# Performance work log

Measured on AMD Instinct MI355X. Metric: run time of the kernel, lower is better.

## Reference

```python
import jax, jax.numpy as jnp
import numpy as np

D_MODEL = 256
N_HEADS = 4
WINDOW = 8
DECAY = 0.9
STEP_SIZE = 0.5


def _linear(x, w, b):
    # torch nn.Linear: y = x @ w.T + b, w: [out, in]
    return jnp.einsum('...i,oi->...o', x, w) + b


def _layernorm(x, scale, bias, eps=1e-5):
    mu = jnp.mean(x, axis=-1, keepdims=True)
    var = jnp.var(x, axis=-1, keepdims=True)
    return (x - mu) * jax.lax.rsqrt(var + eps) * scale + bias


def _ema(x, decay):
    # ema[t] = decay*ema[t-1] + (1-decay)*x[t], ema[-1]=0
    # (exactly the causal conv with weights (1-d)*d^i from the torch code)
    def step(c, xt):
        c = decay * c + (1.0 - decay) * xt
        return c, c
    _, ys = jax.lax.scan(step, jnp.zeros_like(x[:, 0]), jnp.swapaxes(x, 0, 1))
    return jnp.swapaxes(ys, 0, 1)


def setup_inputs() -> dict:
    key = jax.random.key(0)
    ks = iter(jax.random.split(key, 40))
    B, T, D = 8, 1024, D_MODEL
    s = 0.02
    inp = {
        'parallel_repr': jax.random.normal(next(ks), (B, T, D), jnp.float32),
        'sequential_state': jax.random.normal(next(ks), (B, D), jnp.float32),
        'trajectory_summary': jax.random.normal(next(ks), (B, D), jnp.float32),
        # MultiheadAttention params
        'in_proj_w': jax.random.normal(next(ks), (3 * D, D), jnp.float32) * s,
        'in_proj_b': jnp.zeros((3 * D,), jnp.float32),
        'out_proj_w': jax.random.normal(next(ks), (D, D), jnp.float32) * s,
        'out_proj_b': jnp.zeros((D,), jnp.float32),
        # depthwise causal conv (local history)
        'conv_w': jax.random.normal(next(ks), (D, 1, WINDOW), jnp.float32) * s,
        'conv_b': jnp.zeros((D,), jnp.float32),
        # parallel_to_sequential / sequential_to_parallel
        'p2s_w': jax.random.normal(next(ks), (D, D), jnp.float32) * s,
        'p2s_b': jnp.zeros((D,), jnp.float32),
        's2p_w': jax.random.normal(next(ks), (D, D), jnp.float32) * s,
        's2p_b': jnp.zeros((D,), jnp.float32),
        # transition MLP: 3D -> 2D -> D
        'trans_w1': jax.random.normal(next(ks), (2 * D, 3 * D), jnp.float32) * s,
        'trans_b1': jnp.zeros((2 * D,), jnp.float32),
        'trans_w2': jax.random.normal(next(ks), (D, 2 * D), jnp.float32) * s,
        'trans_b2': jnp.zeros((D,), jnp.float32),
        # FFN: D -> 4D -> D
        'ffn_w1': jax.random.normal(next(ks), (4 * D, D), jnp.float32) * s,
        'ffn_b1': jnp.zeros((4 * D,), jnp.float32),
        'ffn_w2': jax.random.normal(next(ks), (D, 4 * D), jnp.float32) * s,
        'ffn_b2': jnp.zeros((D,), jnp.float32),
        # LayerNorms
        'ln1_s': jnp.ones((D,), jnp.float32), 'ln1_b': jnp.zeros((D,), jnp.float32),
        'ln2_s': jnp.ones((D,), jnp.float32), 'ln2_b': jnp.zeros((D,), jnp.float32),
        'ln3_s': jnp.ones((D,), jnp.float32), 'ln3_b': jnp.zeros((D,), jnp.float32),
        'ln4_s': jnp.ones((D,), jnp.float32), 'ln4_b': jnp.zeros((D,), jnp.float32),
    }
    return inp


def _forward(parallel_repr, sequential_state,
             in_proj_w, in_proj_b, out_proj_w, out_proj_b,
             conv_w, conv_b, p2s_w, p2s_b, s2p_w, s2p_b,
             trans_w1, trans_b1, trans_w2, trans_b2,
             ffn_w1, ffn_b1, ffn_w2, ffn_b2,
             ln1_s, ln1_b, ln2_s, ln2_b, ln3_s, ln3_b, ln4_s, ln4_b):
    B, T, D = parallel_repr.shape
    H, hd = N_HEADS, D // N_HEADS

    # --- causal self-attention (nn.MultiheadAttention, batch_first) ---
    qkv = _linear(parallel_repr, in_proj_w, in_proj_b)
    q, k, v = jnp.split(qkv, 3, axis=-1)
    q = q.reshape(B, T, H, hd)
    k = k.reshape(B, T, H, hd)
    v = v.reshape(B, T, H, hd)
    scores = jnp.einsum('bqhd,bkhd->bhqk', q, k) / jnp.sqrt(jnp.asarray(hd, q.dtype))
    causal = jnp.triu(jnp.ones((T, T), bool), 1)
    scores = jnp.where(causal, jnp.finfo(scores.dtype).min, scores)
    attn = jax.nn.softmax(scores, axis=-1)
    attn_out = jnp.einsum('bhqk,bkhd->bqhd', attn, v).reshape(B, T, D)
    attn_out = _linear(attn_out, out_proj_w, out_proj_b)
    x = _layernorm(parallel_repr + attn_out, ln1_s, ln1_b)

    # --- depthwise causal conv (local history) ---
    xt = jnp.swapaxes(x, 1, 2)  # [B, D, T]
    xt_pad = jnp.pad(xt, ((0, 0), (0, 0), (WINDOW - 1, 0)))
    local = jax.lax.conv_general_dilated(
        xt_pad, conv_w, window_strides=(1,), padding='VALID',
        dimension_numbers=('NCH', 'OIH', 'NCH'), feature_group_count=D)
    local_history = jnp.swapaxes(local + conv_b[None, :, None], 1, 2)  # [B, T, D]

    # --- global EMA summary ---
    global_summary = _ema(x, DECAY)

    # --- transition deltas + cumsum state integration ---
    parallel_guidance = _linear(x, p2s_w, p2s_b)
    combined = jnp.concatenate([x + 0.3 * parallel_guidance, local_history, global_summary], axis=-1)
    h = jax.nn.gelu(_linear(combined, trans_w1, trans_b1), approximate=False)
    deltas = _linear(h, trans_w2, trans_b2)
    states = sequential_state[:, None, :] + jnp.cumsum(deltas, axis=1) * STEP_SIZE
    states = _layernorm(states, ln3_s, ln3_b)

    # --- FFN with sequential guidance ---
    seq_guidance = _linear(states, s2p_w, s2p_b)
    f = jax.nn.gelu(_linear(x + 0.3 * seq_guidance, ffn_w1, ffn_b1), approximate=False)
    ffn_out = _linear(f, ffn_w2, ffn_b2)
    x = _layernorm(x + ffn_out, ln2_s, ln2_b)

    final_sequential_state = _layernorm(states[:, -1, :], ln4_s, ln4_b)
    final_trajectory_summary = global_summary[:, -1, :]
    return x, final_sequential_state, final_trajectory_summary


def reference(parallel_repr, sequential_state, trajectory_summary,
              in_proj_w, in_proj_b, out_proj_w, out_proj_b,
              conv_w, conv_b, p2s_w, p2s_b, s2p_w, s2p_b,
              trans_w1, trans_b1, trans_w2, trans_b2,
              ffn_w1, ffn_b1, ffn_w2, ffn_b2,
              ln1_s, ln1_b, ln2_s, ln2_b, ln3_s, ln3_b, ln4_s, ln4_b):
    # trajectory_summary is accepted by the torch forward but never used.
    return _forward(parallel_repr, sequential_state,
                    in_proj_w, in_proj_b, out_proj_w, out_proj_b,
                    conv_w, conv_b, p2s_w, p2s_b, s2p_w, s2p_b,
                    trans_w1, trans_b1, trans_w2, trans_b2,
                    ffn_w1, ffn_b1, ffn_w2, ffn_b2,
                    ln1_s, ln1_b, ln2_s, ln2_b, ln3_s, ln3_b, ln4_s, ln4_b)
```

## Files before the change

kernel.cpp:

```cpp
#include <hip/hip_runtime.h>
#include <math.h>

typedef unsigned short u16;
typedef __attribute__((ext_vector_type(8))) short bf16x8;
typedef __attribute__((ext_vector_type(4))) float f32x4;

#define D_MODEL 256
#define T_SZ 1024
constexpr size_t S_ELT = (size_t)8192 * 256;
constexpr size_t MB = 1024 * 1024;

constexpr size_t OFF_QKV = 0;
constexpr size_t OFF_ATTN = 12 * MB;
constexpr size_t OFF_F = 0;
constexpr size_t OFF_X = 16 * MB;
constexpr size_t OFF_COMB = 24 * MB;
constexpr size_t OFF_FB = 36 * MB;
constexpr size_t OFF_H = 44 * MB;
constexpr size_t OFF_XBF = 48 * MB;
constexpr size_t OFF_WB = 52 * MB;
constexpr size_t OFF_SCR1 = 55 * MB;
constexpr size_t OFF_SCR2 = 55 * MB + 262144;

constexpr int WB_INPROJ = 0;
constexpr int WB_OUTPROJ = 196608;
constexpr int WB_P2S = 262144;
constexpr int WB_S2P = 327680;
constexpr int WB_T1 = 393216;
constexpr int WB_T2 = 786432;
constexpr int WB_F1 = 917504;
constexpr int WB_F2 = 1179648;
constexpr int WB_TOTAL = 1441792;

__device__ __forceinline__ u16 f2bf(float f) {
  unsigned int u = __float_as_uint(f);
  u += 0x7fff + ((u >> 16) & 1);
  return (u16)(u >> 16);
}
__device__ __forceinline__ float bf2f(u16 s) {
  return __uint_as_float(((unsigned int)s) << 16);
}

__device__ __forceinline__ void glds16(const u16* g, u16* l) {
  __builtin_amdgcn_global_load_lds(
      (const __attribute__((address_space(1))) void*)g,
      (__attribute__((address_space(3))) void*)l, 16, 0, 0);
}

__global__ __launch_bounds__(256)
void wconv_kernel(const float* w0, const float* w1, const float* w2,
                  const float* w3, const float* w4, const float* w5,
                  const float* w6, const float* w7, u16* __restrict__ outp) {
  const int idx4 = (blockIdx.x * 256 + threadIdx.x) * 4;
  if (idx4 >= WB_TOTAL) return;
  const int offs[9] = {WB_INPROJ, WB_OUTPROJ, WB_P2S,  WB_S2P, WB_T1,
                       WB_T2,     WB_F1,      WB_F2,   WB_TOTAL};
  const float* srcs[8] = {w0, w1, w2, w3, w4, w5, w6, w7};
  int seg = 0;
  while (idx4 >= offs[seg + 1]) ++seg;
  float4 v = *(const float4*)(srcs[seg] + (idx4 - offs[seg]));
  unsigned int lo = (unsigned int)f2bf(v.x) | ((unsigned int)f2bf(v.y) << 16);
  unsigned int hi = (unsigned int)f2bf(v.z) | ((unsigned int)f2bf(v.w) << 16);
  *(uint2*)(outp + idx4) = make_uint2(lo, hi);
}

__global__ __launch_bounds__(256)
void cvtbf_kernel(const float* __restrict__ src, u16* __restrict__ dst) {
  const int i4 = (blockIdx.x * 256 + threadIdx.x) * 4;
  float4 v = *(const float4*)(src + i4);
  unsigned int lo = (unsigned int)f2bf(v.x) | ((unsigned int)f2bf(v.y) << 16);
  unsigned int hi = (unsigned int)f2bf(v.z) | ((unsigned int)f2bf(v.w) << 16);
  *(uint2*)(dst + i4) = make_uint2(lo, hi);
}

enum { EPI_NONE = 0, EPI_GELU = 1, EPI_ADDSCALE = 2 };

template <int EPI, int BM, int BN, bool OUTBF>
__global__ __launch_bounds__(256)
void mgemm(const u16* __restrict__ A, int lda,
           const u16* __restrict__ Wb, int K, const float* __restrict__ bias,
           void* __restrict__ Cv, int ldc, int col_off,
           const float* __restrict__ addsrc) {
  __shared__ u16 As[BM * 32];
  __shared__ u16 Bs[BN * 32];
  const int tid = threadIdx.x;
  const int w = tid >> 6, lane = tid & 63;
  const int ln = lane & 15, quad = lane >> 4;
  const int m0 = blockIdx.x * BM;
  const int n0 = blockIdx.y * BN;
  constexpr int MT = (BM == 128 && BN == 128) ? 4 : (BM == 128 ? 2 : 1);
  const int wm = (BM == 128 && BN == 128) ? (w >> 1) * 64
                 : (BM == 128)            ? w * 32
                                          : w * 16;
  const int wn = (BM == 128 && BN == 128) ? (w & 1) * 64 : 0;
  constexpr int APW = BM / 64;
  constexpr int BPW = BN / 64;

  f32x4 acc[MT][4] = {};

  const int grow = lane >> 2;
  const int gk8 = (lane & 3) * 8;

  for (int k0 = 0; k0 < K; k0 += 32) {
#pragma unroll
    for (int p = 0; p < APW; ++p) {
      const int g = w * APW + p;
      glds16(A + (size_t)(m0 + g * 16 + grow) * lda + k0 + gk8, As + g * 512);
    }
#pragma unroll
    for (int p = 0; p < BPW; ++p) {
      const int g = w * BPW + p;
      glds16(Wb + (size_t)(n0 + g * 16 + grow) * K + k0 + gk8, Bs + g * 512);
    }
    __syncthreads();

    const u16* abase = As + (wm >> 4) * 512 + ln * 32 + quad * 8;
    const u16* bbase = Bs + (wn >> 4) * 512 + ln * 32 + quad * 8;
    bf16x8 af[MT], bv[4];
#pragma unroll
    for (int i = 0; i < MT; ++i) af[i] = *(const bf16x8*)(abase + i * 512);
#pragma unroll
    for (int j = 0; j < 4; ++j) bv[j] = *(const bf16x8*)(bbase + j * 512);
#pragma unroll
    for (int i = 0; i < MT; ++i)
#pragma unroll
      for (int j = 0; j < 4; ++j)
        acc[i][j] =
            __builtin_amdgcn_mfma_f32_16x16x32_bf16(af[i], bv[j], acc[i][j], 0, 0, 0);
    __syncthreads();
  }

#pragma unroll
  for (int i = 0; i < MT; ++i)
#pragma unroll
    for (int j = 0; j < 4; ++j) {
      const int col = n0 + wn + j * 16 + ln;
      const float bsv = bias[col];
#pragma unroll
      for (int r = 0; r < 4; ++r) {
        const int row = m0 + wm + i * 16 + quad * 4 + r;
        float v = acc[i][j][r] + bsv;
        if (EPI == EPI_GELU) v = 0.5f * v * (1.0f + erff(v * 0.70710678f));
        if (EPI == EPI_ADDSCALE) v = addsrc[(size_t)row * 256 + col] + 0.3f * v;
        if (OUTBF)
          ((u16*)Cv)[(size_t)row * ldc + col_off + col] = f2bf(v);
        else
          ((float*)Cv)[(size_t)row * ldc + col_off + col] = v;
      }
    }
}

__global__ __launch_bounds__(256)
void vtr_kernel(const u16* __restrict__ qkv, u16* __restrict__ vt) {
  __shared__ u16 Ls[64][66];
  const int tid = threadIdx.x;
  const int t0 = blockIdx.x * 64;
  const int bh = blockIdx.y;
  const int b = bh >> 2, h = bh & 3;
  const int r0 = tid >> 3, c8 = (tid & 7) * 8;
#pragma unroll
  for (int p = 0; p < 2; ++p) {
    const int t = t0 + r0 + p * 32;
    *(uint4*)&Ls[r0 + p * 32][c8] =
        *(const uint4*)(qkv + (size_t)(b * T_SZ + t) * 768 + 512 + h * 64 + c8);
  }
  __syncthreads();
#pragma unroll
  for (int p = 0; p < 2; ++p) {
    const int d = r0 + p * 32;
    union { u16 h16[8]; uint4 u; } pk;
#pragma unroll
    for (int e = 0; e < 8; ++e) pk.h16[e] = Ls[c8 + e][d];
    *(uint4*)(vt + (size_t)(bh * 64 + d) * T_SZ + t0 + c8) = pk.u;
  }
}

__global__ __launch_bounds__(256)
void attn_flash(const u16* __restrict__ qkv, const u16* __restrict__ vt,
                u16* __restrict__ outp) {
  __shared__ u16 Ps[4][16][72];
  const int tid = threadIdx.x;
  const int w = tid >> 6, lane = tid & 63;
  const int ln = lane & 15, quad = lane >> 4, kq8 = quad * 8;
  const int wu = blockIdx.x * 4 + w;
  const int bh = wu >> 6, s = wu & 63;
  const int qt = (s & 1) ? (63 - (s >> 1)) : (s >> 1);
  const int q0 = qt * 16;
  const int b = bh >> 2, h = bh & 3;
  const u16* base = qkv + (size_t)b * T_SZ * 768;
  const u16* vbase = vt + (size_t)bh * 64 * T_SZ;

  bf16x8 qf[2];
#pragma unroll
  for (int ks = 0; ks < 2; ++ks)
    qf[ks] = *(const bf16x8*)(base + (size_t)(q0 + ln) * 768 + h * 64 +
                              ks * 32 + kq8);
  const short ob = (short)0x3F80;
  const bf16x8 ones = {ob, ob, ob, ob, ob, ob, ob, ob};

  f32x4 O[4] = {};
  f32x4 l_acc = {};
  const int ntiles = (qt >> 2) + 1;
  for (int jt = 0; jt < ntiles; ++jt) {
    const int c0 = jt * 64;
    f32x4 sv[4] = {};
#pragma unroll
    for (int ks = 0; ks < 2; ++ks)
#pragma unroll
      for (int j = 0; j < 4; ++j) {
        bf16x8 kf = *(const bf16x8*)(base + (size_t)(c0 + j * 16 + ln) * 768 +
                                     256 + h * 64 + ks * 32 + kq8);
        sv[j] = __builtin_amdgcn_mfma_f32_16x16x32_bf16(qf[ks], kf, sv[j], 0, 0, 0);
      }
    const bool need_mask = (c0 + 63 > q0);
#pragma unroll
    for (int j = 0; j < 4; ++j)
#pragma unroll
      for (int r = 0; r < 4; ++r) {
        float p = __expf(sv[j][r] * 0.125f);
        if (need_mask && (c0 + j * 16 + ln > q0 + quad * 4 + r)) p = 0.f;
        Ps[w][quad * 4 + r][j * 16 + ln] = f2bf(p);
      }
#pragma unroll
    for (int ks = 0; ks < 2; ++ks) {
      bf16x8 pf = *(const bf16x8*)&Ps[w][ln][ks * 32 + kq8];
      l_acc = __builtin_amdgcn_mfma_f32_16x16x32_bf16(pf, ones, l_acc, 0, 0, 0);
#pragma unroll
      for (int j = 0; j < 4; ++j) {
        bf16x8 vf = *(const bf16x8*)(vbase + (size_t)(j * 16 + ln) * T_SZ +
                                     c0 + ks * 32 + kq8);
        O[j] = __builtin_amdgcn_mfma_f32_16x16x32_bf16(pf, vf, O[j], 0, 0, 0);
      }
    }
  }
  u16* op = outp + (size_t)b * T_SZ * 256;
#pragma unroll
  for (int r = 0; r < 4; ++r) {
    const float inv = 1.f / l_acc[r];
#pragma unroll
    for (int j = 0; j < 4; ++j)
      op[(size_t)(q0 + quad * 4 + r) * 256 + h * 64 + j * 16 + ln] =
          f2bf(O[j][r] * inv);
  }
}

__device__ __forceinline__ float block_reduce_sum(float v, float* tmp) {
#pragma unroll
  for (int o = 32; o > 0; o >>= 1) v += __shfl_down(v, o);
  const int lane = threadIdx.x & 63, wid = threadIdx.x >> 6;
  if (lane == 0) tmp[wid] = v;
  __syncthreads();
  v = tmp[0] + tmp[1] + tmp[2] + tmp[3];
  __syncthreads();
  return v;
}

__device__ __forceinline__ float ln_finish(float v, float s1, float s2,
                                           float g, float bb) {
  float mean = s1 * (1.f / 256.f);
  float var = s2 * (1.f / 256.f) - mean * mean;
  return (v - mean) * rsqrtf(var + 1e-5f) * g + bb;
}

__global__ __launch_bounds__(256)
void ln_add_kernel(const float* __restrict__ a, const float* __restrict__ addsrc,
                   const float* __restrict__ g, const float* __restrict__ bb,
                   float* __restrict__ outp, u16* __restrict__ obf) {
  __shared__ float tmp[4];
  const size_t row = blockIdx.x;
  const int d = threadIdx.x;
  float v = a[row * 256 + d] + addsrc[row * 256 + d];
  float s1 = block_reduce_sum(v, tmp);
  float s2 = block_reduce_sum(v * v, tmp);
  float y = ln_finish(v, s1, s2, g[d], bb[d]);
  outp[row * 256 + d] = y;
  if (obf) obf[row * 256 + d] = f2bf(y);
}

__global__ __launch_bounds__(256)
void ln3_states_kernel(const float* __restrict__ deltas, const float* __restrict__ scr,
                       const float* __restrict__ seq, const float* __restrict__ g,
                       const float* __restrict__ bb, u16* __restrict__ st) {
  __shared__ float tmp[4];
  const int row = blockIdx.x;
  const int b = row >> 10, t = row & 1023;
  const int d = threadIdx.x;
  float v = seq[b * 256 + d] +
            0.5f * (deltas[(size_t)row * 256 + d] +
                    scr[(size_t)(b * 32 + (t >> 5)) * 256 + d]);
  float s1 = block_reduce_sum(v, tmp);
  float s2 = block_reduce_sum(v * v, tmp);
  st[(size_t)row * 256 + d] = f2bf(ln_finish(v, s1, s2, g[d], bb[d]));
}

__global__ __launch_bounds__(256)
void ln4_kernel(const u16* __restrict__ st, const float* __restrict__ g,
                const float* __restrict__ bb, float* __restrict__ outp) {
  __shared__ float tmp[4];
  const int b = blockIdx.x, d = threadIdx.x;
  float v = bf2f(st[(size_t)(b * T_SZ + 1023) * 256 + d]);
  float s1 = block_reduce_sum(v, tmp);
  float s2 = block_reduce_sum(v * v, tmp);
  outp[b * 256 + d] = ln_finish(v, s1, s2, g[d], bb[d]);
}

__global__ __launch_bounds__(256)
void emaconv_kernel(const float* __restrict__ x, const float* __restrict__ cw,
                    const float* __restrict__ cb, u16* __restrict__ comb,
                    float* __restrict__ scr) {
  const int bc = blockIdx.x;
  const int b = bc >> 5, ch = bc & 31;
  const int d = threadIdx.x;
  const int t0 = ch * 32;
  float wreg[8];
#pragma unroll
  for (int j = 0; j < 8; ++j) wreg[j] = cw[d * 8 + j];
  const float bias = cb[d];
  float xw[8];
#pragma unroll
  for (int j = 0; j < 7; ++j) {
    const int ts = t0 - 7 + j;
    xw[j] = (ts >= 0) ? x[(size_t)(b * T_SZ + ts) * 256 + d] : 0.f;
  }
  float c = 0.f;
#pragma unroll
  for (int tl = 0; tl < 32; ++tl) {
    const size_t row = (size_t)(b * T_SZ + t0 + tl);
    xw[7] = x[row * 256 + d];
    float conv = bias;
#pragma unroll
    for (int j = 0; j < 8; ++j) conv = fmaf(xw[j], wreg[j], conv);
    c = 0.9f * c + 0.1f * xw[7];
    comb[row * 768 + 256 + d] = f2bf(conv);
    comb[row * 768 + 512 + d] = f2bf(c);
#pragma unroll
    for (int j = 0; j < 7; ++j) xw[j] = xw[j + 1];
  }
  scr[(size_t)bc * 256 + d] = c;
}

__global__ __launch_bounds__(256)
void ema_b_kernel(float* __restrict__ scr) {
  const int b = blockIdx.x, d = threadIdx.x;
  const float q32 = 0.03433683820292512f;
  float carry = 0.f;
  for (int ch = 0; ch < 32; ++ch) {
    const size_t idx = (size_t)(b * 32 + ch) * 256 + d;
    float e = scr[idx];
    scr[idx] = carry;
    carry = e + q32 * carry;
  }
}

__global__ __launch_bounds__(256)
void ema_c_kernel(u16* __restrict__ comb, const float* __restrict__ scr,
                  float* __restrict__ fts) {
  const int row = blockIdx.x;
  const int b = row >> 10, t = row & 1023;
  const int d = threadIdx.x;
  const int ch = t >> 5, tl = t & 31;
  float carry = scr[(size_t)(b * 32 + ch) * 256 + d];
  float l = bf2f(comb[(size_t)row * 768 + 512 + d]);
  float y = fmaf(__powf(0.9f, (float)(tl + 1)), carry, l);
  comb[(size_t)row * 768 + 512 + d] = f2bf(y);
  if (t == 1023) fts[b * 256 + d] = y;
}

__global__ __launch_bounds__(256)
void cs_a_kernel(float* __restrict__ deltas, float* __restrict__ scr) {
  const int bc = blockIdx.x;
  const int b = bc >> 5, ch = bc & 31;
  const int d = threadIdx.x;
  const int t0 = ch * 32;
  float c = 0.f;
  for (int tl = 0; tl < 32; ++tl) {
    const size_t idx = (size_t)(b * T_SZ + t0 + tl) * 256 + d;
    c += deltas[idx];
    deltas[idx] = c;
  }
  scr[(size_t)bc * 256 + d] = c;
}

__global__ __launch_bounds__(256)
void cs_b_kernel(float* __restrict__ scr) {
  const int b = blockIdx.x, d = threadIdx.x;
  float carry = 0.f;
  for (int ch = 0; ch < 32; ++ch) {
    const size_t idx = (size_t)(b * 32 + ch) * 256 + d;
    float e = scr[idx];
    scr[idx] = carry;
    carry += e;
  }
}

extern "C" void kernel_launch(void* const* d_in, const int* in_sizes, int n_in,
                              void* d_out, int out_size, void* d_ws,
                              size_t ws_size, hipStream_t stream) {
  (void)in_sizes; (void)n_in; (void)out_size; (void)ws_size;
  const float* parallel_repr = (const float*)d_in[0];
  const float* sequential_state = (const float*)d_in[1];
  const float* in_proj_b = (const float*)d_in[4];
  const float* out_proj_b = (const float*)d_in[6];
  const float* conv_w = (const float*)d_in[7];
  const float* conv_b = (const float*)d_in[8];
  const float* p2s_b = (const float*)d_in[10];
  const float* s2p_b = (const float*)d_in[12];
  const float* trans_b1 = (const float*)d_in[14];
  const float* trans_b2 = (const float*)d_in[16];
  const float* ffn_b1 = (const float*)d_in[18];
  const float* ffn_b2 = (const float*)d_in[20];
  const float* ln1_s = (const float*)d_in[21];
  const float* ln1_b = (const float*)d_in[22];
  const float* ln2_s = (const float*)d_in[23];
  const float* ln2_b = (const float*)d_in[24];
  const float* ln3_s = (const float*)d_in[25];
  const float* ln3_b = (const float*)d_in[26];
  const float* ln4_s = (const float*)d_in[27];
  const float* ln4_b = (const float*)d_in[28];

  char* ws = (char*)d_ws;
  u16* qkv_bf = (u16*)(ws + OFF_QKV);
  u16* attn_bf = (u16*)(ws + OFF_ATTN);
  u16* states_bf = (u16*)(ws + OFF_ATTN);
  u16* f_bf = (u16*)(ws + OFF_F);
  float* x = (float*)(ws + OFF_X);
  u16* comb = (u16*)(ws + OFF_COMB);
  u16* pr_bf = (u16*)(ws + OFF_COMB);
  u16* ffn_in = (u16*)(ws + OFF_COMB);
  float* fbuf = (float*)(ws + OFF_FB);
  u16* vt = (u16*)(ws + OFF_H);
  u16* h_bf = (u16*)(ws + OFF_H);
  u16* x_bf = (u16*)(ws + OFF_XBF);
  u16* wb = (u16*)(ws + OFF_WB);
  float* scr1 = (float*)(ws + OFF_SCR1);
  float* scr2 = (float*)(ws + OFF_SCR2);
  float* out = (float*)d_out;
  float* out_fss = out + S_ELT;
  float* out_fts = out + S_ELT + 2048;

  const dim3 blk(256);

  wconv_kernel<<<1408, blk, 0, stream>>>(
      (const float*)d_in[3], (const float*)d_in[5], (const float*)d_in[9],
      (const float*)d_in[11], (const float*)d_in[13], (const float*)d_in[15],
      (const float*)d_in[17], (const float*)d_in[19], wb);
  cvtbf_kernel<<<2048, blk, 0, stream>>>(parallel_repr, pr_bf);
  mgemm<EPI_NONE, 128, 128, true><<<dim3(64, 6), blk, 0, stream>>>(
      pr_bf, 256, wb + WB_INPROJ, 256, in_proj_b, qkv_bf, 768, 0, nullptr);
  vtr_kernel<<<dim3(16, 32), blk, 0, stream>>>(qkv_bf, vt);
  attn_flash<<<512, blk, 0, stream>>>(qkv_bf, vt, attn_bf);
  mgemm<EPI_NONE, 64, 64, false><<<dim3(128, 4), blk, 0, stream>>>(
      attn_bf, 256, wb + WB_OUTPROJ, 256, out_proj_b, fbuf, 256, 0, nullptr);
  ln_add_kernel<<<8192, blk, 0, stream>>>(parallel_repr, fbuf, ln1_s, ln1_b, x,
                                          x_bf);
  emaconv_kernel<<<256, blk, 0, stream>>>(x, conv_w, conv_b, comb, scr1);
  ema_b_kernel<<<8, blk, 0, stream>>>(scr1);
  ema_c_kernel<<<8192, blk, 0, stream>>>(comb, scr1, out_fts);
  mgemm<EPI_ADDSCALE, 64, 64, true><<<dim3(128, 4), blk, 0, stream>>>(
      x_bf, 256, wb + WB_P2S, 256, p2s_b, comb, 768, 0, x);
  mgemm<EPI_GELU, 128, 128, true><<<dim3(64, 4), blk, 0, stream>>>(
      comb, 768, wb + WB_T1, 768, trans_b1, h_bf, 512, 0, nullptr);
  mgemm<EPI_NONE, 64, 64, false><<<dim3(128, 4), blk, 0, stream>>>(
      h_bf, 512, wb + WB_T2, 512, trans_b2, fbuf, 256, 0, nullptr);
  cs_a_kernel<<<256, blk, 0, stream>>>(fbuf, scr2);
  cs_b_kernel<<<8, blk, 0, stream>>>(scr2);
  ln3_states_kernel<<<8192, blk, 0, stream>>>(fbuf, scr2, sequential_state,
                                              ln3_s, ln3_b, states_bf);
  ln4_kernel<<<8, blk, 0, stream>>>(states_bf, ln4_s, ln4_b, out_fss);
  mgemm<EPI_ADDSCALE, 64, 64, true><<<dim3(128, 4), blk, 0, stream>>>(
      states_bf, 256, wb + WB_S2P, 256, s2p_b, ffn_in, 256, 0, x);
  mgemm<EPI_GELU, 128, 128, true><<<dim3(64, 8), blk, 0, stream>>>(
      ffn_in, 256, wb + WB_F1, 256, ffn_b1, f_bf, 1024, 0, nullptr);
  mgemm<EPI_NONE, 64, 64, false><<<dim3(128, 4), blk, 0, stream>>>(
      f_bf, 1024, wb + WB_F2, 1024, ffn_b2, fbuf, 256, 0, nullptr);
  ln_add_kernel<<<8192, blk, 0, stream>>>(x, fbuf, ln2_s, ln2_b, out, nullptr);
}
```

Before: 303.3 us.

## Fuse conversions, write V transposed from QKV GEMM, deepen K tile

Merges the weight and input bf16 conversion kernels into one launch. The QKV GEMM epilogue now writes the V columns straight into the transposed layout, which removes the separate transpose kernel. The GEMM now stages K=64 per barrier instead of 32, halving the number of synchronisations, and drops the 128x128 tile in favour of 128x64 with more blocks and a min-occupancy launch bound. The transposed V store is a strided 8-byte write, so it may coalesce less well than the old transpose kernel, and the doubled LDS tiles can limit occupancy.

```diff
diff --git a/kernel.cpp b/kernel.cpp
--- a/kernel.cpp
+++ b/kernel.cpp
@@ -31,6 +31,7 @@
 constexpr int WB_F1 = 917504;
 constexpr int WB_F2 = 1179648;
 constexpr int WB_TOTAL = 1441792;
+constexpr int PR_TOTAL = 2097152;
 
 __device__ __forceinline__ u16 f2bf(float f) {
   unsigned int u = __float_as_uint(f);
@@ -50,49 +51,48 @@
 __global__ __launch_bounds__(256)
 void wconv_kernel(const float* w0, const float* w1, const float* w2,
                   const float* w3, const float* w4, const float* w5,
-                  const float* w6, const float* w7, u16* __restrict__ outp) {
+                  const float* w6, const float* w7, const float* pr,
+                  u16* __restrict__ wb, u16* __restrict__ prb) {
   const int idx4 = (blockIdx.x * 256 + threadIdx.x) * 4;
-  if (idx4 >= WB_TOTAL) return;
-  const int offs[9] = {WB_INPROJ, WB_OUTPROJ, WB_P2S,  WB_S2P, WB_T1,
-                       WB_T2,     WB_F1,      WB_F2,   WB_TOTAL};
-  const float* srcs[8] = {w0, w1, w2, w3, w4, w5, w6, w7};
-  int seg = 0;
-  while (idx4 >= offs[seg + 1]) ++seg;
-  float4 v = *(const float4*)(srcs[seg] + (idx4 - offs[seg]));
-  unsigned int lo = (unsigned int)f2bf(v.x) | ((unsigned int)f2bf(v.y) << 16);
-  unsigned int hi = (unsigned int)f2bf(v.z) | ((unsigned int)f2bf(v.w) << 16);
-  *(uint2*)(outp + idx4) = make_uint2(lo, hi);
-}
-
-__global__ __launch_bounds__(256)
-void cvtbf_kernel(const float* __restrict__ src, u16* __restrict__ dst) {
-  const int i4 = (blockIdx.x * 256 + threadIdx.x) * 4;
-  float4 v = *(const float4*)(src + i4);
-  unsigned int lo = (unsigned int)f2bf(v.x) | ((unsigned int)f2bf(v.y) << 16);
-  unsigned int hi = (unsigned int)f2bf(v.z) | ((unsigned int)f2bf(v.w) << 16);
-  *(uint2*)(dst + i4) = make_uint2(lo, hi);
+  if (idx4 < WB_TOTAL) {
+    const int offs[9] = {WB_INPROJ, WB_OUTPROJ, WB_P2S,  WB_S2P, WB_T1,
+                         WB_T2,     WB_F1,      WB_F2,   WB_TOTAL};
+    const float* srcs[8] = {w0, w1, w2, w3, w4, w5, w6, w7};
+    int seg = 0;
+    while (idx4 >= offs[seg + 1]) ++seg;
+    float4 v = *(const float4*)(srcs[seg] + (idx4 - offs[seg]));
+    unsigned int lo = (unsigned int)f2bf(v.x) | ((unsigned int)f2bf(v.y) << 16);
+    unsigned int hi = (unsigned int)f2bf(v.z) | ((unsigned int)f2bf(v.w) << 16);
+    *(uint2*)(wb + idx4) = make_uint2(lo, hi);
+  } else {
+    const int i4 = idx4 - WB_TOTAL;
+    if (i4 < PR_TOTAL) {
+      float4 v = *(const float4*)(pr + i4);
+      unsigned int lo = (unsigned int)f2bf(v.x) | ((unsigned int)f2bf(v.y) << 16);
+      unsigned int hi = (unsigned int)f2bf(v.z) | ((unsigned int)f2bf(v.w) << 16);
+      *(uint2*)(prb + i4) = make_uint2(lo, hi);
+    }
+  }
 }
 
 enum { EPI_NONE = 0, EPI_GELU = 1, EPI_ADDSCALE = 2 };
 
-template <int EPI, int BM, int BN, bool OUTBF>
-__global__ __launch_bounds__(256)
+template <int EPI, int BM, int BN, bool OUTBF, bool VSPLIT>
+__global__ __launch_bounds__(256, 4)
 void mgemm(const u16* __restrict__ A, int lda,
            const u16* __restrict__ Wb, int K, const float* __restrict__ bias,
            void* __restrict__ Cv, int ldc, int col_off,
-           const float* __restrict__ addsrc) {
-  __shared__ u16 As[BM * 32];
-  __shared__ u16 Bs[BN * 32];
+           const float* __restrict__ addsrc, u16* __restrict__ vt) {
+  __shared__ u16 As[BM * 64];
+  __shared__ u16 Bs[BN * 64];
   const int tid = threadIdx.x;
   const int w = tid >> 6, lane = tid & 63;
   const int ln = lane & 15, quad = lane >> 4;
   const int m0 = blockIdx.x * BM;
   const int n0 = blockIdx.y * BN;
-  constexpr int MT = (BM == 128 && BN == 128) ? 4 : (BM == 128 ? 2 : 1);
-  const int wm = (BM == 128 && BN == 128) ? (w >> 1) * 64
-                 : (BM == 128)            ? w * 32
-                                          : w * 16;
-  const int wn = (BM == 128 && BN == 128) ? (w & 1) * 64 : 0;
+  constexpr int MT = (BM == 128) ? 2 : 1;
+  const int wm = w * (MT * 16);
+  constexpr int wn = 0;
   constexpr int APW = BM / 64;
   constexpr int BPW = BN / 64;
 
@@ -101,32 +101,39 @@
   const int grow = lane >> 2;
   const int gk8 = (lane & 3) * 8;
 
-  for (int k0 = 0; k0 < K; k0 += 32) {
-#pragma unroll
-    for (int p = 0; p < APW; ++p) {
-      const int g = w * APW + p;
-      glds16(A + (size_t)(m0 + g * 16 + grow) * lda + k0 + gk8, As + g * 512);
-    }
-#pragma unroll
-    for (int p = 0; p < BPW; ++p) {
-      const int g = w * BPW + p;
-      glds16(Wb + (size_t)(n0 + g * 16 + grow) * K + k0 + gk8, Bs + g * 512);
+  for (int k0 = 0; k0 < K; k0 += 64) {
+#pragma unroll
+    for (int s = 0; s < 2; ++s) {
+#pragma unroll
+      for (int p = 0; p < APW; ++p) {
+        const int g = w * APW + p;
+        glds16(A + (size_t)(m0 + g * 16 + grow) * lda + k0 + s * 32 + gk8,
+               As + s * BM * 32 + g * 512);
+      }
+#pragma unroll
+      for (int p = 0; p < BPW; ++p) {
+        const int g = w * BPW + p;
+        glds16(Wb + (size_t)(n0 + g * 16 + grow) * K + k0 + s * 32 + gk8,
+               Bs + s * BN * 32 + g * 512);
+      }
     }
     __syncthreads();
-
-    const u16* abase = As + (wm >> 4) * 512 + ln * 32 + quad * 8;
-    const u16* bbase = Bs + (wn >> 4) * 512 + ln * 32 + quad * 8;
-    bf16x8 af[MT], bv[4];
-#pragma unroll
-    for (int i = 0; i < MT; ++i) af[i] = *(const bf16x8*)(abase + i * 512);
-#pragma unroll
-    for (int j = 0; j < 4; ++j) bv[j] = *(const bf16x8*)(bbase + j * 512);
-#pragma unroll
-    for (int i = 0; i < MT; ++i)
-#pragma unroll
-      for (int j = 0; j < 4; ++j)
-        acc[i][j] =
-            __builtin_amdgcn_mfma_f32_16x16x32_bf16(af[i], bv[j], acc[i][j], 0, 0, 0);
+#pragma unroll
+    for (int s = 0; s < 2; ++s) {
+      const u16* abase = As + s * BM * 32 + (wm >> 4) * 512 + ln * 32 + quad * 8;
+      const u16* bbase = Bs + s * BN * 32 + ln * 32 + quad * 8;
+      bf16x8 af[MT], bv[4];
+#pragma unroll
+      for (int i = 0; i < MT; ++i) af[i] = *(const bf16x8*)(abase + i * 512);
+#pragma unroll
+      for (int j = 0; j < 4; ++j) bv[j] = *(const bf16x8*)(bbase + j * 512);
+#pragma unroll
+      for (int i = 0; i < MT; ++i)
+#pragma unroll
+        for (int j = 0; j < 4; ++j)
+          acc[i][j] = __builtin_amdgcn_mfma_f32_16x16x32_bf16(af[i], bv[j],
+                                                              acc[i][j], 0, 0, 0);
+    }
     __syncthreads();
   }
 
@@ -136,43 +143,32 @@
     for (int j = 0; j < 4; ++j) {
       const int col = n0 + wn + j * 16 + ln;
       const float bsv = bias[col];
+      const int row0 = m0 + wm + i * 16 + quad * 4;
+      float vals[4];
 #pragma unroll
       for (int r = 0; r < 4; ++r) {
-        const int row = m0 + wm + i * 16 + quad * 4 + r;
         float v = acc[i][j][r] + bsv;
         if (EPI == EPI_GELU) v = 0.5f * v * (1.0f + erff(v * 0.70710678f));
-        if (EPI == EPI_ADDSCALE) v = addsrc[(size_t)row * 256 + col] + 0.3f * v;
-        if (OUTBF)
-          ((u16*)Cv)[(size_t)row * ldc + col_off + col] = f2bf(v);
-        else
-          ((float*)Cv)[(size_t)row * ldc + col_off + col] = v;
+        if (EPI == EPI_ADDSCALE)
+          v = addsrc[(size_t)(row0 + r) * 256 + col] + 0.3f * v;
+        vals[r] = v;
+      }
+      if (VSPLIT && col >= 512) {
+        ushort4 pk;
+        pk.x = f2bf(vals[0]); pk.y = f2bf(vals[1]);
+        pk.z = f2bf(vals[2]); pk.w = f2bf(vals[3]);
+        *(ushort4*)(vt + (size_t)((row0 >> 10) * 256 + (col - 512)) * T_SZ +
+                    (row0 & 1023)) = pk;
+      } else if (OUTBF) {
+#pragma unroll
+        for (int r = 0; r < 4; ++r)
+          ((u16*)Cv)[(size_t)(row0 + r) * ldc + col_off + col] = f2bf(vals[r]);
+      } else {
+#pragma unroll
+        for (int r = 0; r < 4; ++r)
+          ((float*)Cv)[(size_t)(row0 + r) * ldc + col_off + col] = vals[r];
       }
     }
-}
-
-__global__ __launch_bounds__(256)
-void vtr_kernel(const u16* __restrict__ qkv, u16* __restrict__ vt) {
-  __shared__ u16 Ls[64][66];
-  const int tid = threadIdx.x;
-  const int t0 = blockIdx.x * 64;
-  const int bh = blockIdx.y;
-  const int b = bh >> 2, h = bh & 3;
-  const int r0 = tid >> 3, c8 = (tid & 7) * 8;
-#pragma unroll
-  for (int p = 0; p < 2; ++p) {
-    const int t = t0 + r0 + p * 32;
-    *(uint4*)&Ls[r0 + p * 32][c8] =
-        *(const uint4*)(qkv + (size_t)(b * T_SZ + t) * 768 + 512 + h * 64 + c8);
-  }
-  __syncthreads();
-#pragma unroll
-  for (int p = 0; p < 2; ++p) {
-    const int d = r0 + p * 32;
-    union { u16 h16[8]; uint4 u; } pk;
-#pragma unroll
-    for (int e = 0; e < 8; ++e) pk.h16[e] = Ls[c8 + e][d];
-    *(uint4*)(vt + (size_t)(bh * 64 + d) * T_SZ + t0 + c8) = pk.u;
-  }
 }
 
 __global__ __launch_bounds__(256)
@@ -440,38 +436,37 @@
 
   const dim3 blk(256);
 
-  wconv_kernel<<<1408, blk, 0, stream>>>(
+  wconv_kernel<<<3456, blk, 0, stream>>>(
       (const float*)d_in[3], (const float*)d_in[5], (const float*)d_in[9],
       (const float*)d_in[11], (const float*)d_in[13], (const float*)d_in[15],
-      (const float*)d_in[17], (const float*)d_in[19], wb);
-  cvtbf_kernel<<<2048, blk, 0, stream>>>(parallel_repr, pr_bf);
-  mgemm<EPI_NONE, 128, 128, true><<<dim3(64, 6), blk, 0, stream>>>(
-      pr_bf, 256, wb + WB_INPROJ, 256, in_proj_b, qkv_bf, 768, 0, nullptr);
-  vtr_kernel<<<dim3(16, 32), blk, 0, stream>>>(qkv_bf, vt);
+      (const float*)d_in[17], (const float*)d_in[19], parallel_repr, wb, pr_bf);
+  mgemm<EPI_NONE, 128, 64, true, true><<<dim3(64, 12), blk, 0, stream>>>(
+      pr_bf, 256, wb + WB_INPROJ, 256, in_proj_b, qkv_bf, 768, 0, nullptr, vt);
   attn_flash<<<512, blk, 0, stream>>>(qkv_bf, vt, attn_bf);
-  mgemm<EPI_NONE, 64, 64, false><<<dim3(128, 4), blk, 0, stream>>>(
-      attn_bf, 256, wb + WB_OUTPROJ, 256, out_proj_b, fbuf, 256, 0, nullptr);
+  mgemm<EPI_NONE, 64, 64, false, false><<<dim3(128, 4), blk, 0, stream>>>(
+      attn_bf, 256, wb + WB_OUTPROJ, 256, out_proj_b, fbuf, 256, 0, nullptr,
+      nullptr);
   ln_add_kernel<<<8192, blk, 0, stream>>>(parallel_repr, fbuf, ln1_s, ln1_b, x,
                                           x_bf);
   emaconv_kernel<<<256, blk, 0, stream>>>(x, conv_w, conv_b, comb, scr1);
   ema_b_kernel<<<8, blk, 0, stream>>>(scr1);
   ema_c_kernel<<<8192, blk, 0, stream>>>(comb, scr1, out_fts);
-  mgemm<EPI_ADDSCALE, 64, 64, true><<<dim3(128, 4), blk, 0, stream>>>(
-      x_bf, 256, wb + WB_P2S, 256, p2s_b, comb, 768, 0, x);
-  mgemm<EPI_GELU, 128, 128, true><<<dim3(64, 4), blk, 0, stream>>>(
-      comb, 768, wb + WB_T1, 768, trans_b1, h_bf, 512, 0, nullptr);
-  mgemm<EPI_NONE, 64, 64, false><<<dim3(128, 4), blk, 0, stream>>>(
-      h_bf, 512, wb + WB_T2, 512, trans_b2, fbuf, 256, 0, nullptr);
+  mgemm<EPI_ADDSCALE, 64, 64, true, false><<<dim3(128, 4), blk, 0, stream>>>(
+      x_bf, 256, wb + WB_P2S, 256, p2s_b, comb, 768, 0, x, nullptr);
+  mgemm<EPI_GELU, 128, 64, true, false><<<dim3(64, 8), blk, 0, stream>>>(
+      comb, 768, wb + WB_T1, 768, trans_b1, h_bf, 512, 0, nullptr, nullptr);
+  mgemm<EPI_NONE, 64, 64, false, false><<<dim3(128, 4), blk, 0, stream>>>(
+      h_bf, 512, wb + WB_T2, 512, trans_b2, fbuf, 256, 0, nullptr, nullptr);
   cs_a_kernel<<<256, blk, 0, stream>>>(fbuf, scr2);
   cs_b_kernel<<<8, blk, 0, stream>>>(scr2);
   ln3_states_kernel<<<8192, blk, 0, stream>>>(fbuf, scr2, sequential_state,
                                               ln3_s, ln3_b, states_bf);
   ln4_kernel<<<8, blk, 0, stream>>>(states_bf, ln4_s, ln4_b, out_fss);
-  mgemm<EPI_ADDSCALE, 64, 64, true><<<dim3(128, 4), blk, 0, stream>>>(
-      states_bf, 256, wb + WB_S2P, 256, s2p_b, ffn_in, 256, 0, x);
-  mgemm<EPI_GELU, 128, 128, true><<<dim3(64, 8), blk, 0, stream>>>(
-      ffn_in, 256, wb + WB_F1, 256, ffn_b1, f_bf, 1024, 0, nullptr);
-  mgemm<EPI_NONE, 64, 64, false><<<dim3(128, 4), blk, 0, stream>>>(
-      f_bf, 1024, wb + WB_F2, 1024, ffn_b2, fbuf, 256, 0, nullptr);
+  mgemm<EPI_ADDSCALE, 64, 64, true, false><<<dim3(128, 4), blk, 0, stream>>>(
+      states_bf, 256, wb + WB_S2P, 256, s2p_b, ffn_in, 256, 0, x, nullptr);
+  mgemm<EPI_GELU, 128, 64, true, false><<<dim3(64, 16), blk, 0, stream>>>(
+      ffn_in, 256, wb + WB_F1, 256, ffn_b1, f_bf, 1024, 0, nullptr, nullptr);
+  mgemm<EPI_NONE, 64, 64, false, false><<<dim3(128, 4), blk, 0, stream>>>(
+      f_bf, 1024, wb + WB_F2, 1024, ffn_b2, fbuf, 256, 0, nullptr, nullptr);
   ln_add_kernel<<<8192, blk, 0, stream>>>(x, fbuf, ln2_s, ln2_b, out, nullptr);
 }
```

Result: faster. 276.3 us (-8.9%).
